# Performance work log

Hardware: AMD Instinct MI355X
Metric: run time of the kernel (lower is better)

The kernel has to match this reference:

```python
import jax, jax.numpy as jnp
import numpy as np

NUM_HEADS = 16
LN_EPS = 1e-05


def setup_inputs() -> dict:
    key = jax.random.key(0)
    ks = jax.random.split(key, 10)
    B, S, H = 2, 2048, 1024
    s = 1.0 / np.sqrt(H)
    return {
        "hidden_states": jax.random.normal(ks[0], (B, S, H), dtype=jnp.float32),
        "Wq": jax.random.normal(ks[1], (H, H), dtype=jnp.float32) * s,
        "bq": jax.random.normal(ks[2], (H,), dtype=jnp.float32) * 0.02,
        "Wk": jax.random.normal(ks[3], (H, H), dtype=jnp.float32) * s,
        "bk": jax.random.normal(ks[4], (H,), dtype=jnp.float32) * 0.02,
        "Wv": jax.random.normal(ks[5], (H, H), dtype=jnp.float32) * s,
        "bv": jax.random.normal(ks[6], (H,), dtype=jnp.float32) * 0.02,
        "Wd": jax.random.normal(ks[7], (H, H), dtype=jnp.float32) * s,
        "bd": jax.random.normal(ks[8], (H,), dtype=jnp.float32) * 0.02,
        "ln_gamma": jnp.ones((H,), dtype=jnp.float32),
        "ln_beta": jnp.zeros((H,), dtype=jnp.float32),
    }


def reference(hidden_states, Wq, bq, Wk, bk, Wv, bv, Wd, bd, ln_gamma, ln_beta):
    B, S, H = hidden_states.shape
    nh = NUM_HEADS
    hd = H // nh

    # QKV projections (torch Linear: x @ W.T + b), split heads -> [B, nh, S, hd]
    def proj(W, b):
        y = jnp.einsum('bsh,oh->bso', hidden_states, W) + b
        return y.reshape(B, S, nh, hd).transpose(0, 2, 1, 3)

    q = proj(Wq, bq)
    k = proj(Wk, bk)
    v = proj(Wv, bv)

    # scaled dot-product attention: [B, nh, S, S]
    scores = jnp.einsum('bhqd,bhkd->bhqk', q, k) / jnp.sqrt(jnp.float32(hd))
    probs = jax.nn.softmax(scores, axis=-1)
    ctx = jnp.einsum('bhqk,bhkd->bhqd', probs, v)  # [B, nh, S, hd]
    ctx = ctx.transpose(0, 2, 1, 3).reshape(B, S, H)

    # output dense + residual + LayerNorm
    attn_out = jnp.einsum('bsh,oh->bso', ctx, Wd) + bd
    x = attn_out + hidden_states
    mu = jnp.mean(x, axis=-1, keepdims=True)
    var = jnp.mean(jnp.square(x - mu), axis=-1, keepdims=True)
    return (x - mu) * jax.lax.rsqrt(var + LN_EPS) * ln_gamma + ln_beta
```

## Files before the change

kernel.cpp:

```cpp
#include <hip/hip_runtime.h>

constexpr int kH    = 1024;
constexpr int kSEQ  = 2048;
constexpr int kBATCH= 2;
constexpr int kNH   = 16;
constexpr int kHD   = 64;
constexpr int kM    = 4096;

typedef _Float16 h8  __attribute__((ext_vector_type(8)));
typedef _Float16 h4  __attribute__((ext_vector_type(4)));
typedef float   f32x4 __attribute__((ext_vector_type(4)));

static __device__ __forceinline__ f32x4 mfma16(h8 a, h8 b, f32x4 c) {
  return __builtin_amdgcn_mfma_f32_16x16x32_f16(a, b, c, 0, 0, 0);
}

static __device__ __forceinline__ void gll16(const _Float16* g, _Float16* l) {
  __builtin_amdgcn_global_load_lds(
      (const __attribute__((address_space(1))) void*)g,
      (__attribute__((address_space(3))) void*)l, 16, 0, 0);
}

#define QSCALE 0.18033688011112042f
#define C0INIT (-5.770780163555854f)

__global__ __launch_bounds__(256) void cvt_all(
    const float* __restrict__ X,  const float* __restrict__ Wq,
    const float* __restrict__ Wk, const float* __restrict__ Wv,
    const float* __restrict__ Wd,
    _Float16* __restrict__ Xh,  _Float16* __restrict__ Wqh,
    _Float16* __restrict__ Wkh, _Float16* __restrict__ Wvh,
    _Float16* __restrict__ Wdh)
{
  int i = blockIdx.x * 256 + threadIdx.x;
  const float* src; _Float16* dst; int off;
  if (i < (kM * kH) / 4) {
    src = X; dst = Xh; off = i;
  } else {
    int j = i - (kM * kH) / 4;
    int w = j >> 18;
    off = j & 262143;
    src = (w == 0) ? Wq : (w == 1) ? Wk : (w == 2) ? Wv : Wd;
    dst = (w == 0) ? Wqh : (w == 1) ? Wkh : (w == 2) ? Wvh : Wdh;
  }
  float4 v = reinterpret_cast<const float4*>(src)[off];
  h4 o;
  o[0] = (_Float16)v.x; o[1] = (_Float16)v.y;
  o[2] = (_Float16)v.z; o[3] = (_Float16)v.w;
  reinterpret_cast<h4*>(dst)[off] = o;
}

__global__ __launch_bounds__(256, 2) void qkv_gemm(
    const _Float16* __restrict__ Xh,
    const _Float16* __restrict__ Wq, const _Float16* __restrict__ Wk,
    const _Float16* __restrict__ Wv,
    const float* __restrict__ bq, const float* __restrict__ bk,
    const float* __restrict__ bv,
    _Float16* __restrict__ Qo, _Float16* __restrict__ Ko, _Float16* __restrict__ Vo)
{
  const int proj = blockIdx.z;
  const _Float16* W   = (proj == 0) ? Wq : ((proj == 1) ? Wk : Wv);
  const float*    bias= (proj == 0) ? bq : ((proj == 1) ? bk : bv);
  _Float16*       Out = (proj == 0) ? Qo : ((proj == 1) ? Ko : Vo);

  const int m0 = blockIdx.y * 128, n0 = blockIdx.x * 128;
  __shared__ __align__(16) _Float16 As[2][128 * 32];
  __shared__ __align__(16) _Float16 Bs[2][128 * 32];

  const int tid  = threadIdx.x;
  const int wave = tid >> 6, lane = tid & 63, quad = lane >> 4, l16 = lane & 15;
  const int mw = (wave & 1) * 64, nw = (wave >> 1) * 64;

  f32x4 acc[4][4] = {};
  const int grow = wave * 32 + (lane >> 2);
  const int gcol = (lane & 3) * 8;
  const _Float16* Ag = Xh + (size_t)(m0 + grow) * kH + gcol;
  const _Float16* Bg = W  + (size_t)(n0 + grow) * kH + gcol;

  {
    gll16(Ag,            &As[0][wave * 1024]);
    gll16(Ag + 16 * kH,  &As[0][wave * 1024 + 512]);
    gll16(Bg,            &Bs[0][wave * 1024]);
    gll16(Bg + 16 * kH,  &Bs[0][wave * 1024 + 512]);
  }

  for (int k = 0; k < 32; ++k) {
    const int cur = k & 1;
    __syncthreads();
    if (k < 31) {
      const int k0 = (k + 1) * 32, nb = cur ^ 1;
      gll16(Ag + k0,           &As[nb][wave * 1024]);
      gll16(Ag + 16 * kH + k0, &As[nb][wave * 1024 + 512]);
      gll16(Bg + k0,           &Bs[nb][wave * 1024]);
      gll16(Bg + 16 * kH + k0, &Bs[nb][wave * 1024 + 512]);
    }
    h8 af[4], bf[4];
    #pragma unroll
    for (int mi = 0; mi < 4; ++mi)
      af[mi] = *reinterpret_cast<const h8*>(&As[cur][(mw + mi * 16 + l16) * 32 + quad * 8]);
    #pragma unroll
    for (int ni = 0; ni < 4; ++ni)
      bf[ni] = *reinterpret_cast<const h8*>(&Bs[cur][(nw + ni * 16 + l16) * 32 + quad * 8]);
    #pragma unroll
    for (int mi = 0; mi < 4; ++mi)
      #pragma unroll
      for (int ni = 0; ni < 4; ++ni)
        acc[mi][ni] = mfma16(af[mi], bf[ni], acc[mi][ni]);
  }

  #pragma unroll
  for (int mi = 0; mi < 4; ++mi)
  #pragma unroll
  for (int ni = 0; ni < 4; ++ni) {
    const int ng = n0 + nw + ni * 16 + l16;
    const float bv_ = bias[ng];
    const int hh = ng >> 6, dd = ng & 63;
    #pragma unroll
    for (int r = 0; r < 4; ++r) {
      const int mg = m0 + mw + mi * 16 + quad * 4 + r;
      float val = acc[mi][ni][r] + bv_;
      if (proj == 0) val *= QSCALE;
      const int bb = mg >> 11, srow = mg & 2047;
      Out[(((size_t)(bb * kNH + hh) * kSEQ) + srow) * kHD + dd] = (_Float16)val;
    }
  }
}

__global__ __launch_bounds__(256) void vtrans(const _Float16* __restrict__ V,
                                              _Float16* __restrict__ Vt)
{
  const int st = blockIdx.x;
  const int bh = blockIdx.y;
  __shared__ __align__(16) _Float16 Lt[64][72];
  const int t = threadIdx.x, r = t >> 2, c = (t & 3) * 16;
  const _Float16* src = V + (size_t)bh * kSEQ * kHD + (size_t)(st * 64 + r) * kHD + c;
  h8 p0 = *reinterpret_cast<const h8*>(src);
  h8 p1 = *reinterpret_cast<const h8*>(src + 8);
  #pragma unroll
  for (int e = 0; e < 8; ++e) Lt[c + e][r] = p0[e];
  #pragma unroll
  for (int e = 0; e < 8; ++e) Lt[c + 8 + e][r] = p1[e];
  __syncthreads();
  _Float16* dst = Vt + (size_t)bh * kHD * kSEQ + (size_t)r * kSEQ + st * 64 + c;
  *reinterpret_cast<h8*>(dst)     = *reinterpret_cast<const h8*>(&Lt[r][c]);
  *reinterpret_cast<h8*>(dst + 8) = *reinterpret_cast<const h8*>(&Lt[r][c + 8]);
}

__global__ __launch_bounds__(512, 4) void attn_kernel(
    const _Float16* __restrict__ Q, const _Float16* __restrict__ K,
    const _Float16* __restrict__ Vt, _Float16* __restrict__ Ctx)
{
  const int qt = blockIdx.x, bh = blockIdx.y;
  const int tid = threadIdx.x;
  const int wave = tid >> 6, lane = tid & 63, quad = lane >> 4, l16 = lane & 15;
  const int sw = l16 & 7;
  const int qw = wave & 3;
  const int wg = wave >> 2;

  __shared__ __align__(16) char smem[53248];
  _Float16* const Kl = (_Float16*)smem;
  _Float16* const Vl = (_Float16*)(smem + 16384);
  _Float16* const Pl = (_Float16*)(smem + 32768);
  float* const Ored = (float*)smem;
  float* const Lred = (float*)(smem + 34816);

  const _Float16* Qb = Q  + (size_t)bh * kSEQ * kHD;
  const _Float16* Kb = K  + (size_t)bh * kSEQ * kHD;
  const _Float16* Vb = Vt + (size_t)bh * kHD * kSEQ;

  const int qbase = qt * 128 + qw * 32;
  h8 qf[2][2];
  #pragma unroll
  for (int qh = 0; qh < 2; ++qh)
    #pragma unroll
    for (int dh = 0; dh < 2; ++dh)
      qf[qh][dh] = *reinterpret_cast<const h8*>(
          &Qb[(size_t)(qbase + qh * 16 + l16) * kHD + dh * 32 + quad * 8]);

  const int srow0  = lane >> 3;
  const int schunk = (lane & 7) ^ srow0;
  const int krow   = wave * 8 + srow0;
  const _Float16* Kg = Kb + (size_t)krow * kHD + schunk * 8;
  const _Float16* Vg = Vb + (size_t)krow * kSEQ + schunk * 8;
  _Float16* const PlW = Pl + wave * 1280;

  float l_acc[2] = {0.f, 0.f};
  f32x4 o[2][4] = {};

  gll16(Kg, &Kl[(wave * 8) * 64]);
  gll16(Vg, &Vl[(wave * 8) * 64]);

  for (int kt = 0; kt < kSEQ / 64; ++kt) {
    const int cur = kt & 1;
    __syncthreads();
    if (kt + 1 < kSEQ / 64) {
      const int nb = cur ^ 1;
      const size_t ko = (size_t)(kt + 1) * 64;
      gll16(Kg + ko * kHD, &Kl[nb * 4096 + (wave * 8) * 64]);
      gll16(Vg + ko,       &Vl[nb * 4096 + (wave * 8) * 64]);
    }
    const _Float16* Kc = Kl + cur * 4096;
    const _Float16* Vc = Vl + cur * 4096;

    h8 ka[2][2];
    #pragma unroll
    for (int nt = 0; nt < 2; ++nt) {
      const int keyl = wg * 32 + nt * 16 + l16;
      ka[nt][0] = *reinterpret_cast<const h8*>(&Kc[keyl * 64 + ((quad    ) ^ sw) * 8]);
      ka[nt][1] = *reinterpret_cast<const h8*>(&Kc[keyl * 64 + ((quad ^ 4) ^ sw) * 8]);
    }
    f32x4 s[2][2];
    __builtin_amdgcn_s_setprio(1);
    #pragma unroll
    for (int nt = 0; nt < 2; ++nt)
      #pragma unroll
      for (int qh = 0; qh < 2; ++qh) {
        f32x4 a = {C0INIT, C0INIT, C0INIT, C0INIT};
        a = mfma16(ka[nt][0], qf[qh][0], a);
        a = mfma16(ka[nt][1], qf[qh][1], a);
        s[nt][qh] = a;
      }
    __builtin_amdgcn_s_setprio(0);

    #pragma unroll
    for (int nt = 0; nt < 2; ++nt)
      #pragma unroll
      for (int qh = 0; qh < 2; ++qh) {
        float e0 = exp2f(s[nt][qh][0]);
        float e1 = exp2f(s[nt][qh][1]);
        float e2 = exp2f(s[nt][qh][2]);
        float e3 = exp2f(s[nt][qh][3]);
        l_acc[qh] += (e0 + e1) + (e2 + e3);
        h4 pp;
        pp[0] = (_Float16)e0; pp[1] = (_Float16)e1;
        pp[2] = (_Float16)e2; pp[3] = (_Float16)e3;
        const int c = nt * 2 + (quad >> 1);
        *reinterpret_cast<h4*>(&PlW[(qh * 16 + l16) * 40 + c * 8 + (quad & 1) * 4]) = pp;
      }

    h8 pa0 = *reinterpret_cast<const h8*>(&PlW[(     l16) * 40 + quad * 8]);
    h8 pa1 = *reinterpret_cast<const h8*>(&PlW[(16 + l16) * 40 + quad * 8]);
    const int cs = ((wg * 4 + quad) ^ sw) * 8;
    h8 vb0 = *reinterpret_cast<const h8*>(&Vc[(0 * 16 + l16) * 64 + cs]);
    h8 vb1 = *reinterpret_cast<const h8*>(&Vc[(1 * 16 + l16) * 64 + cs]);
    h8 vb2 = *reinterpret_cast<const h8*>(&Vc[(2 * 16 + l16) * 64 + cs]);
    h8 vb3 = *reinterpret_cast<const h8*>(&Vc[(3 * 16 + l16) * 64 + cs]);
    __builtin_amdgcn_s_setprio(1);
    o[0][0] = mfma16(pa0, vb0, o[0][0]);
    o[1][0] = mfma16(pa1, vb0, o[1][0]);
    o[0][1] = mfma16(pa0, vb1, o[0][1]);
    o[1][1] = mfma16(pa1, vb1, o[1][1]);
    o[0][2] = mfma16(pa0, vb2, o[0][2]);
    o[1][2] = mfma16(pa1, vb2, o[1][2]);
    o[0][3] = mfma16(pa0, vb3, o[0][3]);
    o[1][3] = mfma16(pa1, vb3, o[1][3]);
    __builtin_amdgcn_s_setprio(0);
  }

  float li[2] = {l_acc[0], l_acc[1]};
  #pragma unroll
  for (int qh = 0; qh < 2; ++qh) {
    li[qh] += __shfl_xor(li[qh], 16);
    li[qh] += __shfl_xor(li[qh], 32);
  }

  __syncthreads();
  if (wg == 1) {
    float* myO = Ored + (qw * 64 + lane) * 34;
    #pragma unroll
    for (int qh = 0; qh < 2; ++qh)
      #pragma unroll
      for (int dt = 0; dt < 4; ++dt) {
        reinterpret_cast<float2*>(&myO[qh * 16 + dt * 4])[0] =
            reinterpret_cast<const float2*>(&o[qh][dt])[0];
        reinterpret_cast<float2*>(&myO[qh * 16 + dt * 4 + 2])[0] =
            reinterpret_cast<const float2*>(&o[qh][dt])[1];
      }
    if (quad == 0) {
      Lred[(qw * 2 + 0) * 16 + l16] = li[0];
      Lred[(qw * 2 + 1) * 16 + l16] = li[1];
    }
  }
  __syncthreads();
  if (wg == 1) return;

  const float* pO = Ored + (qw * 64 + lane) * 34;
  #pragma unroll
  for (int qh = 0; qh < 2; ++qh) {
    #pragma unroll
    for (int dt = 0; dt < 4; ++dt) {
      float2 a = reinterpret_cast<const float2*>(&pO[qh * 16 + dt * 4])[0];
      float2 b2 = reinterpret_cast<const float2*>(&pO[qh * 16 + dt * 4 + 2])[0];
      o[qh][dt][0] += a.x;  o[qh][dt][1] += a.y;
      o[qh][dt][2] += b2.x; o[qh][dt][3] += b2.y;
    }
    li[qh] = 1.f / (li[qh] + Lred[(qw * 2 + qh) * 16 + l16]);
  }
  const int b = bh >> 4, hh = bh & 15;
  #pragma unroll
  for (int qh = 0; qh < 2; ++qh)
    #pragma unroll
    for (int r = 0; r < 4; ++r) {
      const float linv = __shfl(li[qh], quad * 4 + r);
      const int srow = qbase + qh * 16 + quad * 4 + r;
      #pragma unroll
      for (int dt = 0; dt < 4; ++dt) {
        const int col = hh * kHD + dt * 16 + l16;
        Ctx[((size_t)(b * kSEQ + srow)) * kH + col] = (_Float16)(o[qh][dt][r] * linv);
      }
    }
}

__global__ __launch_bounds__(256, 2) void dense_gemm(
    const _Float16* __restrict__ A, const _Float16* __restrict__ W,
    const float* __restrict__ bias, const float* __restrict__ resid,
    float* __restrict__ Out)
{
  const int m0 = blockIdx.y * 128, n0 = blockIdx.x * 64;
  __shared__ __align__(16) _Float16 As[2][128 * 32];
  __shared__ __align__(16) _Float16 Bs[2][64 * 32];
  const int tid  = threadIdx.x;
  const int wave = tid >> 6, lane = tid & 63, quad = lane >> 4, l16 = lane & 15;
  const int mw = (wave & 1) * 64, nw = (wave >> 1) * 32;
  f32x4 acc[4][2] = {};
  const int growA = wave * 32 + (lane >> 2);
  const int growB = wave * 16 + (lane >> 2);
  const int gcol = (lane & 3) * 8;
  const _Float16* Ag = A + (size_t)(m0 + growA) * kH + gcol;
  const _Float16* Bg = W + (size_t)(n0 + growB) * kH + gcol;

  {
    gll16(Ag,           &As[0][wave * 1024]);
    gll16(Ag + 16 * kH, &As[0][wave * 1024 + 512]);
    gll16(Bg,           &Bs[0][wave * 512]);
  }

  for (int k = 0; k < 32; ++k) {
    const int cur = k & 1;
    __syncthreads();
    if (k < 31) {
      const int k0 = (k + 1) * 32, nb = cur ^ 1;
      gll16(Ag + k0,           &As[nb][wave * 1024]);
      gll16(Ag + 16 * kH + k0, &As[nb][wave * 1024 + 512]);
      gll16(Bg + k0,           &Bs[nb][wave * 512]);
    }
    h8 af[4], bf[2];
    #pragma unroll
    for (int mi = 0; mi < 4; ++mi)
      af[mi] = *reinterpret_cast<const h8*>(&As[cur][(mw + mi * 16 + l16) * 32 + quad * 8]);
    #pragma unroll
    for (int ni = 0; ni < 2; ++ni)
      bf[ni] = *reinterpret_cast<const h8*>(&Bs[cur][(nw + ni * 16 + l16) * 32 + quad * 8]);
    #pragma unroll
    for (int mi = 0; mi < 4; ++mi)
      #pragma unroll
      for (int ni = 0; ni < 2; ++ni)
        acc[mi][ni] = mfma16(af[mi], bf[ni], acc[mi][ni]);
  }
  #pragma unroll
  for (int mi = 0; mi < 4; ++mi)
  #pragma unroll
  for (int ni = 0; ni < 2; ++ni) {
    const int ng = n0 + nw + ni * 16 + l16;
    const float bv_ = bias[ng];
    #pragma unroll
    for (int r = 0; r < 4; ++r) {
      const int mg = m0 + mw + mi * 16 + quad * 4 + r;
      Out[(size_t)mg * kH + ng] = acc[mi][ni][r] + bv_ + resid[(size_t)mg * kH + ng];
    }
  }
}

__global__ __launch_bounds__(256) void ln_kernel(const float* __restrict__ Tmp,
    const float* __restrict__ gamma, const float* __restrict__ beta,
    float* __restrict__ out)
{
  const int row = blockIdx.x;
  const float4 v = reinterpret_cast<const float4*>(Tmp + (size_t)row * kH)[threadIdx.x];
  float s  = v.x + v.y + v.z + v.w;
  float ss = v.x * v.x + v.y * v.y + v.z * v.z + v.w * v.w;
  #pragma unroll
  for (int off = 32; off > 0; off >>= 1) {
    s  += __shfl_down(s, off);
    ss += __shfl_down(ss, off);
  }
  __shared__ float red[8];
  const int wave = threadIdx.x >> 6, lane = threadIdx.x & 63;
  if (lane == 0) { red[wave] = s; red[4 + wave] = ss; }
  __syncthreads();
  s  = red[0] + red[1] + red[2] + red[3];
  ss = red[4] + red[5] + red[6] + red[7];
  const float mu   = s * (1.f / kH);
  const float var  = ss * (1.f / kH) - mu * mu;
  const float rstd = rsqrtf(var + 1e-5f);
  const float4 g  = reinterpret_cast<const float4*>(gamma)[threadIdx.x];
  const float4 bb = reinterpret_cast<const float4*>(beta)[threadIdx.x];
  float4 o;
  o.x = (v.x - mu) * rstd * g.x + bb.x;
  o.y = (v.y - mu) * rstd * g.y + bb.y;
  o.z = (v.z - mu) * rstd * g.z + bb.z;
  o.w = (v.w - mu) * rstd * g.w + bb.w;
  reinterpret_cast<float4*>(out + (size_t)row * kH)[threadIdx.x] = o;
}

extern "C" void kernel_launch(void* const* d_in, const int* in_sizes, int n_in,
                              void* d_out, int out_size, void* d_ws, size_t ws_size,
                              hipStream_t stream) {
  const float* hs    = (const float*)d_in[0];
  const float* Wq    = (const float*)d_in[1];
  const float* bq    = (const float*)d_in[2];
  const float* Wk    = (const float*)d_in[3];
  const float* bk    = (const float*)d_in[4];
  const float* Wv    = (const float*)d_in[5];
  const float* bv    = (const float*)d_in[6];
  const float* Wd    = (const float*)d_in[7];
  const float* bd    = (const float*)d_in[8];
  const float* gamma = (const float*)d_in[9];
  const float* beta  = (const float*)d_in[10];
  float* out = (float*)d_out;

  char* ws = (char*)d_ws;
  _Float16* Xh  = (_Float16*)(ws + 0);
  _Float16* Wqh = (_Float16*)(ws + 8388608);
  _Float16* Wkh = (_Float16*)(ws + 10485760);
  _Float16* Wvh = (_Float16*)(ws + 12582912);
  _Float16* Wdh = (_Float16*)(ws + 14680064);
  _Float16* Qh  = (_Float16*)(ws + 16777216);
  _Float16* Kh  = (_Float16*)(ws + 25165824);
  _Float16* Vh  = (_Float16*)(ws + 33554432);
  _Float16* Ch  = (_Float16*)(ws + 41943040);
  _Float16* Vtb = Xh;
  float*    Tmp = (float*)Qh;

  cvt_all<<<8192, 256, 0, stream>>>(hs, Wq, Wk, Wv, Wd, Xh, Wqh, Wkh, Wvh, Wdh);
  qkv_gemm<<<dim3(kH / 128, kM / 128, 3), 256, 0, stream>>>(
      Xh, Wqh, Wkh, Wvh, bq, bk, bv, Qh, Kh, Vh);
  vtrans<<<dim3(kSEQ / 64, kBATCH * kNH), 256, 0, stream>>>(Vh, Vtb);
  attn_kernel<<<dim3(kSEQ / 128, kBATCH * kNH), 512, 0, stream>>>(Qh, Kh, Vtb, Ch);
  dense_gemm<<<dim3(kH / 64, kM / 128), 256, 0, stream>>>(Ch, Wdh, bd, hs, Tmp);
  ln_kernel<<<kM, 256, 0, stream>>>(Tmp, gamma, beta, out);
}
```

Measured before the change: 218.5 us.

## Fuse V transpose into QKV GEMM epilogue, swizzle P tile, use native exp2

The V projection epilogue now stages its tile in shared memory with an XOR swizzle and writes V already transposed ([d][seq]), which removes the separate vtrans kernel launch and its extra round trip through global memory. The attention kernel also XOR-swizzles the P staging buffer to reduce LDS bank conflicts and switches exp2f to the hardware builtin. The costs are an extra barrier and LDS staging in the V-block epilogue, and slightly different exp2 precision at the extremes.

```diff
diff --git a/kernel.cpp b/kernel.cpp
--- a/kernel.cpp
+++ b/kernel.cpp
@@ -64,8 +64,10 @@
   _Float16*       Out = (proj == 0) ? Qo : ((proj == 1) ? Ko : Vo);
 
   const int m0 = blockIdx.y * 128, n0 = blockIdx.x * 128;
-  __shared__ __align__(16) _Float16 As[2][128 * 32];
-  __shared__ __align__(16) _Float16 Bs[2][128 * 32];
+  __shared__ __align__(16) char qsmem[32768];
+  _Float16* const As = (_Float16*)qsmem;
+  _Float16* const Bs = (_Float16*)(qsmem + 16384);
+  _Float16* const Lt = (_Float16*)qsmem;
 
   const int tid  = threadIdx.x;
   const int wave = tid >> 6, lane = tid & 63, quad = lane >> 4, l16 = lane & 15;
@@ -78,10 +80,10 @@
   const _Float16* Bg = W  + (size_t)(n0 + grow) * kH + gcol;
 
   {
-    gll16(Ag,            &As[0][wave * 1024]);
-    gll16(Ag + 16 * kH,  &As[0][wave * 1024 + 512]);
-    gll16(Bg,            &Bs[0][wave * 1024]);
-    gll16(Bg + 16 * kH,  &Bs[0][wave * 1024 + 512]);
+    gll16(Ag,            &As[wave * 1024]);
+    gll16(Ag + 16 * kH,  &As[wave * 1024 + 512]);
+    gll16(Bg,            &Bs[wave * 1024]);
+    gll16(Bg + 16 * kH,  &Bs[wave * 1024 + 512]);
   }
 
   for (int k = 0; k < 32; ++k) {
@@ -89,18 +91,18 @@
     __syncthreads();
     if (k < 31) {
       const int k0 = (k + 1) * 32, nb = cur ^ 1;
-      gll16(Ag + k0,           &As[nb][wave * 1024]);
-      gll16(Ag + 16 * kH + k0, &As[nb][wave * 1024 + 512]);
-      gll16(Bg + k0,           &Bs[nb][wave * 1024]);
-      gll16(Bg + 16 * kH + k0, &Bs[nb][wave * 1024 + 512]);
+      gll16(Ag + k0,           &As[nb * 4096 + wave * 1024]);
+      gll16(Ag + 16 * kH + k0, &As[nb * 4096 + wave * 1024 + 512]);
+      gll16(Bg + k0,           &Bs[nb * 4096 + wave * 1024]);
+      gll16(Bg + 16 * kH + k0, &Bs[nb * 4096 + wave * 1024 + 512]);
     }
     h8 af[4], bf[4];
     #pragma unroll
     for (int mi = 0; mi < 4; ++mi)
-      af[mi] = *reinterpret_cast<const h8*>(&As[cur][(mw + mi * 16 + l16) * 32 + quad * 8]);
+      af[mi] = *reinterpret_cast<const h8*>(&As[cur * 4096 + (mw + mi * 16 + l16) * 32 + quad * 8]);
     #pragma unroll
     for (int ni = 0; ni < 4; ++ni)
-      bf[ni] = *reinterpret_cast<const h8*>(&Bs[cur][(nw + ni * 16 + l16) * 32 + quad * 8]);
+      bf[ni] = *reinterpret_cast<const h8*>(&Bs[cur * 4096 + (nw + ni * 16 + l16) * 32 + quad * 8]);
     #pragma unroll
     for (int mi = 0; mi < 4; ++mi)
       #pragma unroll
@@ -108,42 +110,55 @@
         acc[mi][ni] = mfma16(af[mi], bf[ni], acc[mi][ni]);
   }
 
-  #pragma unroll
-  for (int mi = 0; mi < 4; ++mi)
-  #pragma unroll
-  for (int ni = 0; ni < 4; ++ni) {
-    const int ng = n0 + nw + ni * 16 + l16;
-    const float bv_ = bias[ng];
-    const int hh = ng >> 6, dd = ng & 63;
-    #pragma unroll
-    for (int r = 0; r < 4; ++r) {
-      const int mg = m0 + mw + mi * 16 + quad * 4 + r;
-      float val = acc[mi][ni][r] + bv_;
-      if (proj == 0) val *= QSCALE;
-      const int bb = mg >> 11, srow = mg & 2047;
-      Out[(((size_t)(bb * kNH + hh) * kSEQ) + srow) * kHD + dd] = (_Float16)val;
-    }
-  }
-}
-
-__global__ __launch_bounds__(256) void vtrans(const _Float16* __restrict__ V,
-                                              _Float16* __restrict__ Vt)
-{
-  const int st = blockIdx.x;
-  const int bh = blockIdx.y;
-  __shared__ __align__(16) _Float16 Lt[64][72];
-  const int t = threadIdx.x, r = t >> 2, c = (t & 3) * 16;
-  const _Float16* src = V + (size_t)bh * kSEQ * kHD + (size_t)(st * 64 + r) * kHD + c;
-  h8 p0 = *reinterpret_cast<const h8*>(src);
-  h8 p1 = *reinterpret_cast<const h8*>(src + 8);
-  #pragma unroll
-  for (int e = 0; e < 8; ++e) Lt[c + e][r] = p0[e];
-  #pragma unroll
-  for (int e = 0; e < 8; ++e) Lt[c + 8 + e][r] = p1[e];
-  __syncthreads();
-  _Float16* dst = Vt + (size_t)bh * kHD * kSEQ + (size_t)r * kSEQ + st * 64 + c;
-  *reinterpret_cast<h8*>(dst)     = *reinterpret_cast<const h8*>(&Lt[r][c]);
-  *reinterpret_cast<h8*>(dst + 8) = *reinterpret_cast<const h8*>(&Lt[r][c + 8]);
+  if (proj != 2) {
+    #pragma unroll
+    for (int mi = 0; mi < 4; ++mi)
+    #pragma unroll
+    for (int ni = 0; ni < 4; ++ni) {
+      const int ng = n0 + nw + ni * 16 + l16;
+      const float bv_ = bias[ng];
+      const int hh = ng >> 6, dd = ng & 63;
+      #pragma unroll
+      for (int r = 0; r < 4; ++r) {
+        const int mg = m0 + mw + mi * 16 + quad * 4 + r;
+        float val = acc[mi][ni][r] + bv_;
+        if (proj == 0) val *= QSCALE;
+        const int bb = mg >> 11, srow = mg & 2047;
+        Out[(((size_t)(bb * kNH + hh) * kSEQ) + srow) * kHD + dd] = (_Float16)val;
+      }
+    }
+  } else {
+    __syncthreads();
+    #pragma unroll
+    for (int mi = 0; mi < 4; ++mi)
+    #pragma unroll
+    for (int ni = 0; ni < 4; ++ni) {
+      const int ng = n0 + nw + ni * 16 + l16;
+      const float bv_ = bias[ng];
+      const int nl = nw + ni * 16 + l16;
+      const int c16 = (mw >> 3) + mi * 2 + (quad >> 1);
+      const int cs = c16 ^ (nl & 15);
+      h4 pp;
+      pp[0] = (_Float16)(acc[mi][ni][0] + bv_);
+      pp[1] = (_Float16)(acc[mi][ni][1] + bv_);
+      pp[2] = (_Float16)(acc[mi][ni][2] + bv_);
+      pp[3] = (_Float16)(acc[mi][ni][3] + bv_);
+      *reinterpret_cast<h4*>(&Lt[nl * 128 + cs * 8 + (quad & 1) * 4]) = pp;
+    }
+    __syncthreads();
+    const int bb = m0 >> 11, srow0 = m0 & 2047;
+    const int nl2 = tid >> 1, half = tid & 1;
+    const int ng2 = n0 + nl2, hh2 = ng2 >> 6, dd2 = ng2 & 63;
+    _Float16* dst = Out + ((size_t)(bb * kNH + hh2) * kHD + dd2) * kSEQ
+                        + srow0 + half * 64;
+    #pragma unroll
+    for (int j = 0; j < 8; ++j) {
+      const int c = half * 8 + j;
+      const int cs = c ^ (nl2 & 15);
+      *reinterpret_cast<h8*>(dst + j * 8) =
+          *reinterpret_cast<const h8*>(&Lt[nl2 * 128 + cs * 8]);
+    }
+  }
 }
 
 __global__ __launch_bounds__(512, 4) void attn_kernel(
@@ -183,6 +198,7 @@
   const _Float16* Kg = Kb + (size_t)krow * kHD + schunk * 8;
   const _Float16* Vg = Vb + (size_t)krow * kSEQ + schunk * 8;
   _Float16* const PlW = Pl + wave * 1280;
+  const int psw = l16 & 3;
 
   float l_acc[2] = {0.f, 0.f};
   f32x4 o[2][4] = {};
@@ -226,20 +242,20 @@
     for (int nt = 0; nt < 2; ++nt)
       #pragma unroll
       for (int qh = 0; qh < 2; ++qh) {
-        float e0 = exp2f(s[nt][qh][0]);
-        float e1 = exp2f(s[nt][qh][1]);
-        float e2 = exp2f(s[nt][qh][2]);
-        float e3 = exp2f(s[nt][qh][3]);
+        float e0 = __builtin_amdgcn_exp2f(s[nt][qh][0]);
+        float e1 = __builtin_amdgcn_exp2f(s[nt][qh][1]);
+        float e2 = __builtin_amdgcn_exp2f(s[nt][qh][2]);
+        float e3 = __builtin_amdgcn_exp2f(s[nt][qh][3]);
         l_acc[qh] += (e0 + e1) + (e2 + e3);
         h4 pp;
         pp[0] = (_Float16)e0; pp[1] = (_Float16)e1;
         pp[2] = (_Float16)e2; pp[3] = (_Float16)e3;
-        const int c = nt * 2 + (quad >> 1);
+        const int c = (nt * 2 + (quad >> 1)) ^ psw;
         *reinterpret_cast<h4*>(&PlW[(qh * 16 + l16) * 40 + c * 8 + (quad & 1) * 4]) = pp;
       }
 
-    h8 pa0 = *reinterpret_cast<const h8*>(&PlW[(     l16) * 40 + quad * 8]);
-    h8 pa1 = *reinterpret_cast<const h8*>(&PlW[(16 + l16) * 40 + quad * 8]);
+    h8 pa0 = *reinterpret_cast<const h8*>(&PlW[(     l16) * 40 + (quad ^ psw) * 8]);
+    h8 pa1 = *reinterpret_cast<const h8*>(&PlW[(16 + l16) * 40 + (quad ^ psw) * 8]);
     const int cs = ((wg * 4 + quad) ^ sw) * 8;
     h8 vb0 = *reinterpret_cast<const h8*>(&Vc[(0 * 16 + l16) * 64 + cs]);
     h8 vb1 = *reinterpret_cast<const h8*>(&Vc[(1 * 16 + l16) * 64 + cs]);
@@ -427,16 +443,14 @@
   _Float16* Wdh = (_Float16*)(ws + 14680064);
   _Float16* Qh  = (_Float16*)(ws + 16777216);
   _Float16* Kh  = (_Float16*)(ws + 25165824);
-  _Float16* Vh  = (_Float16*)(ws + 33554432);
+  _Float16* Vth = (_Float16*)(ws + 33554432);
   _Float16* Ch  = (_Float16*)(ws + 41943040);
-  _Float16* Vtb = Xh;
   float*    Tmp = (float*)Qh;
 
   cvt_all<<<8192, 256, 0, stream>>>(hs, Wq, Wk, Wv, Wd, Xh, Wqh, Wkh, Wvh, Wdh);
   qkv_gemm<<<dim3(kH / 128, kM / 128, 3), 256, 0, stream>>>(
-      Xh, Wqh, Wkh, Wvh, bq, bk, bv, Qh, Kh, Vh);
-  vtrans<<<dim3(kSEQ / 64, kBATCH * kNH), 256, 0, stream>>>(Vh, Vtb);
-  attn_kernel<<<dim3(kSEQ / 128, kBATCH * kNH), 512, 0, stream>>>(Qh, Kh, Vtb, Ch);
+      Xh, Wqh, Wkh, Wvh, bq, bk, bv, Qh, Kh, Vth);
+  attn_kernel<<<dim3(kSEQ / 128, kBATCH * kNH), 512, 0, stream>>>(Qh, Kh, Vth, Ch);
   dense_gemm<<<dim3(kH / 64, kM / 128), 256, 0, stream>>>(Ch, Wdh, bd, hs, Tmp);
   ln_kernel<<<kM, 256, 0, stream>>>(Tmp, gamma, beta, out);
 }
```

Result: faster. 210.7 us (-3.6%).
